# Performance work log

Hardware: AMD Instinct MI355X
Metric: run time of the kernel (lower is better)

The kernel has to match this reference:

```python
import jax, jax.numpy as jnp
import numpy as np

DIM, H, HD = 512, 8, 64
N_BANK = 4096
EPS = 1e-5


def layernorm(x, g, b):
    m = jnp.mean(x, axis=-1, keepdims=True)
    v = jnp.mean(jnp.square(x - m), axis=-1, keepdims=True)
    return (x - m) * jax.lax.rsqrt(v + EPS) * g + b


def setup_inputs() -> dict:
    key = jax.random.key(0)
    ks = jax.random.split(key, 8)
    # xavier_uniform bound for square (512,512) linears
    bound = float(np.sqrt(6.0 / (DIM + DIM)))
    inp = {
        "x_q": jax.random.normal(ks[0], (32, 128, DIM), jnp.float32),
        "x_k": jax.random.normal(ks[1], (N_BANK, DIM), jnp.float32),
        "x_v": jax.random.normal(ks[2], (N_BANK, DIM), jnp.float32),
        "Wq": jax.random.uniform(ks[3], (DIM, DIM), jnp.float32, -bound, bound),
        "Wk": jax.random.uniform(ks[4], (DIM, DIM), jnp.float32, -bound, bound),
        "Wv": jax.random.uniform(ks[5], (DIM, DIM), jnp.float32, -bound, bound),
        "Wproj": jax.random.uniform(ks[6], (DIM, DIM), jnp.float32, -bound, bound),
        "qn_g": jnp.ones((HD,), jnp.float32),
        "qn_b": jnp.zeros((HD,), jnp.float32),
        "kn_g": jnp.ones((HD,), jnp.float32),
        "kn_b": jnp.zeros((HD,), jnp.float32),
        "n_g": jnp.ones((DIM,), jnp.float32),
        "n_b": jnp.zeros((DIM,), jnp.float32),
    }
    return inp


def reference(x_q, x_k, x_v, Wq, Wk, Wv, Wproj, qn_g, qn_b, kn_g, kn_b, n_g, n_b):
    B, S, D = x_q.shape
    N = x_k.shape[0]
    scale = HD ** (-0.5)
    # Linear layers (torch: y = x @ W.T)
    q = jnp.einsum('bsd,od->bso', x_q, Wq).reshape(B, S, H, HD).transpose(0, 2, 1, 3)  # (B,H,S,hd)
    k = jnp.einsum('nd,od->no', x_k, Wk).reshape(N, H, HD).transpose(1, 0, 2)          # (H,N,hd)
    v = jnp.einsum('nd,od->no', x_v, Wv).reshape(N, H, HD).transpose(1, 0, 2)          # (H,N,hd)
    # per-head qk layernorm
    q = layernorm(q, qn_g, qn_b) * scale
    k = layernorm(k, kn_g, kn_b)
    # cross-attention to shared bank (K/V have no batch dim)
    attn = jnp.einsum('bhsd,hnd->bhsn', q, k)          # (B,H,S,N)
    attn = jax.nn.softmax(attn, axis=-1)
    x = jnp.einsum('bhsn,hnd->bhsd', attn, v)          # (B,H,S,hd)
    x = x.transpose(0, 2, 1, 3).reshape(B, S, D)
    x = layernorm(x, n_g, n_b)
    x = jnp.einsum('bsd,od->bso', x, Wproj)
    return x
```

## Files before the change

kernel.cpp:

```cpp
#include <hip/hip_runtime.h>
#include <hip/hip_bf16.h>
#include <math.h>

#define DIM 512
#define NHEAD 8
#define HD 64
#define NBANK 4096
#define NQROWS 4096
#define EPS 1e-5f
#define QSCALE 0.125f
#define PART_ELEMS (NQROWS * DIM)

typedef __attribute__((ext_vector_type(4))) float floatx4;
typedef __attribute__((ext_vector_type(8))) short short8;

__device__ __forceinline__ unsigned short f2bf(float f) {
    unsigned int u = __float_as_uint(f);
    u += 0x7fffu + ((u >> 16) & 1u);
    return (unsigned short)(u >> 16);
}
__device__ __forceinline__ float bf2f(unsigned short h) {
    return __uint_as_float(((unsigned int)h) << 16);
}
__device__ __forceinline__ unsigned int pk2(float a, float b) {
    union { __hip_bfloat162 h; unsigned int u; } cvt;
    cvt.h = __float22bfloat162_rn(make_float2(a, b));
    return cvt.u;
}

__global__ __launch_bounds__(256) void qkv_kernel(
    const float* __restrict__ xq, const float* __restrict__ xk, const float* __restrict__ xv,
    const float* __restrict__ Wqp, const float* __restrict__ Wkp, const float* __restrict__ Wvp,
    const float* __restrict__ qg, const float* __restrict__ qbeta,
    const float* __restrict__ kg, const float* __restrict__ kbeta,
    unsigned short* __restrict__ Qb, unsigned short* __restrict__ Kb,
    unsigned short* __restrict__ VTb)
{
    __shared__ short8 smem[1536];
    short8* as = smem;
    short8* bs = smem + 512;
    const int tid  = threadIdx.x;
    const int w    = tid >> 6, lane = tid & 63, m = lane & 15, q = lane >> 4;
    const int wr   = w & 1, wc = w >> 1;
    const int row0 = blockIdx.x * 64;
    const int mat  = blockIdx.y >> 2;
    const int col0 = (blockIdx.y & 3) * 128;
    const float* X = (mat == 0) ? xq : (mat == 1) ? xk : xv;
    const float* W = (mat == 0) ? Wqp : (mat == 1) ? Wkp : Wvp;

    floatx4 acc[2][4];
    #pragma unroll
    for (int mt = 0; mt < 2; ++mt)
        #pragma unroll
        for (int nt = 0; nt < 4; ++nt) acc[mt][nt] = (floatx4){0.f, 0.f, 0.f, 0.f};

    for (int k0 = 0; k0 < DIM; k0 += 64) {
        #pragma unroll
        for (int p = 0; p < 6; ++p) {
            const int idx = tid + p * 256;
            if (idx < 512) {
                const int row = idx >> 3, seg = idx & 7;
                const float4* pa = (const float4*)(X + (size_t)(row0 + row) * DIM + k0 + seg * 8);
                const float4 a0 = pa[0], a1 = pa[1];
                union { short8 v; unsigned int u[4]; } ta;
                ta.u[0] = pk2(a0.x, a0.y); ta.u[1] = pk2(a0.z, a0.w);
                ta.u[2] = pk2(a1.x, a1.y); ta.u[3] = pk2(a1.z, a1.w);
                as[row * 8 + (seg ^ (row & 7))] = ta.v;
            } else {
                const int j = idx - 512;
                const int row = j >> 3, seg = j & 7;
                const float4* pb = (const float4*)(W + (size_t)(col0 + row) * DIM + k0 + seg * 8);
                const float4 b0 = pb[0], b1 = pb[1];
                union { short8 v; unsigned int u[4]; } tb;
                tb.u[0] = pk2(b0.x, b0.y); tb.u[1] = pk2(b0.z, b0.w);
                tb.u[2] = pk2(b1.x, b1.y); tb.u[3] = pk2(b1.z, b1.w);
                bs[row * 8 + (seg ^ (row & 7))] = tb.v;
            }
        }
        __syncthreads();
        #pragma unroll
        for (int s = 0; s < 2; ++s) {
            short8 af[2], bfr[4];
            #pragma unroll
            for (int mt = 0; mt < 2; ++mt)
                af[mt] = as[(wr * 32 + mt * 16 + m) * 8 + ((s * 4 + q) ^ (m & 7))];
            #pragma unroll
            for (int nt = 0; nt < 4; ++nt)
                bfr[nt] = bs[(wc * 64 + nt * 16 + m) * 8 + ((s * 4 + q) ^ (m & 7))];
            #pragma unroll
            for (int mt = 0; mt < 2; ++mt)
                #pragma unroll
                for (int nt = 0; nt < 4; ++nt)
                    acc[mt][nt] = __builtin_amdgcn_mfma_f32_16x16x32_bf16(af[mt], bfr[nt], acc[mt][nt], 0, 0, 0);
        }
        __syncthreads();
    }

    if (mat < 2) {
        const float* g = (mat == 0) ? qg : kg;
        const float* be = (mat == 0) ? qbeta : kbeta;
        unsigned short* Y = (mat == 0) ? Qb : Kb;
        float gv[4], bv[4];
        #pragma unroll
        for (int nt = 0; nt < 4; ++nt) { gv[nt] = g[nt * 16 + m]; bv[nt] = be[nt * 16 + m]; }
        #pragma unroll
        for (int mt = 0; mt < 2; ++mt) {
            #pragma unroll
            for (int r = 0; r < 4; ++r) {
                float s = 0.f, sq = 0.f;
                #pragma unroll
                for (int nt = 0; nt < 4; ++nt) { const float v = acc[mt][nt][r]; s += v; sq += v * v; }
                s  += __shfl_xor(s, 1);  s  += __shfl_xor(s, 2);  s  += __shfl_xor(s, 4);  s  += __shfl_xor(s, 8);
                sq += __shfl_xor(sq, 1); sq += __shfl_xor(sq, 2); sq += __shfl_xor(sq, 4); sq += __shfl_xor(sq, 8);
                const float mean = s * (1.f / HD);
                const float var  = sq * (1.f / HD) - mean * mean;
                const float rr   = rsqrtf(var + EPS);
                const int grow = row0 + wr * 32 + mt * 16 + q * 4 + r;
                #pragma unroll
                for (int nt = 0; nt < 4; ++nt) {
                    float v = (acc[mt][nt][r] - mean) * rr * gv[nt] + bv[nt];
                    if (mat == 0) v *= QSCALE;
                    Y[(size_t)grow * DIM + col0 + wc * 64 + nt * 16 + m] = f2bf(v);
                }
            }
        }
    } else {
        unsigned short* vt = (unsigned short*)smem;
        #pragma unroll
        for (int mt = 0; mt < 2; ++mt)
            #pragma unroll
            for (int nt = 0; nt < 4; ++nt) {
                const int c  = wc * 64 + nt * 16 + m;
                const int rw = wr * 32 + mt * 16 + q * 4;
                *(unsigned int*)(vt + c * 88 + rw)     = pk2(acc[mt][nt][0], acc[mt][nt][1]);
                *(unsigned int*)(vt + c * 88 + rw + 2) = pk2(acc[mt][nt][2], acc[mt][nt][3]);
            }
        __syncthreads();
        #pragma unroll
        for (int p = 0; p < 4; ++p) {
            const int idx = tid + p * 256;
            const int c = idx >> 3, sg = idx & 7;
            *(short8*)(VTb + (size_t)(col0 + c) * NBANK + row0 + sg * 8) =
                *(const short8*)(vt + c * 88 + sg * 8);
        }
    }
}

__global__ __launch_bounds__(256) void attn_kernel(
    const unsigned short* __restrict__ Qb, const unsigned short* __restrict__ Kb,
    const unsigned short* __restrict__ VTb, unsigned short* __restrict__ AOp,
    float* __restrict__ sums)
{
    __shared__ short8 ks [512];
    __shared__ short8 vts[512];
    __shared__ short8 ps [512];
    const int tid  = threadIdx.x;
    const int w    = tid >> 6;
    const int lane = tid & 63;
    const int m    = lane & 15;
    const int q    = lane >> 4;
    const int h    = blockIdx.x & 7;
    const int row0 = (blockIdx.x >> 3) * 64;
    const int part = blockIdx.y;
    const int base0 = part * 1024;

    short8 qf[2];
    #pragma unroll
    for (int s = 0; s < 2; ++s)
        qf[s] = *(const short8*)(Qb + (size_t)(row0 + w * 16 + m) * DIM + h * HD + s * 32 + q * 8);

    floatx4 of[4];
    float sump[4];
    #pragma unroll
    for (int t = 0; t < 4; ++t) of[t] = (floatx4){0.f, 0.f, 0.f, 0.f};
    #pragma unroll
    for (int r = 0; r < 4; ++r) sump[r] = 0.f;

    unsigned short* psu = (unsigned short*)ps;

    for (int base = base0; base < base0 + 1024; base += 64) {
        __syncthreads();
        #pragma unroll
        for (int it = 0; it < 2; ++it) {
            const int idx = tid + it * 256;
            const int n = idx >> 3, seg = idx & 7, sw = seg ^ (n & 7);
            ks [n * 8 + sw] = *(const short8*)(Kb  + (size_t)(base + n) * DIM  + h * HD + seg * 8);
            vts[n * 8 + sw] = *(const short8*)(VTb + (size_t)(h * HD + n) * NBANK + base + seg * 8);
        }
        __syncthreads();

        floatx4 sc[4];
        #pragma unroll
        for (int t = 0; t < 4; ++t) sc[t] = (floatx4){0.f, 0.f, 0.f, 0.f};
        #pragma unroll
        for (int s = 0; s < 2; ++s) {
            #pragma unroll
            for (int t = 0; t < 4; ++t) {
                const short8 kf = ks[(t * 16 + m) * 8 + ((s * 4 + q) ^ (m & 7))];
                sc[t] = __builtin_amdgcn_mfma_f32_16x16x32_bf16(qf[s], kf, sc[t], 0, 0, 0);
            }
        }

        #pragma unroll
        for (int t = 0; t < 4; ++t) {
            #pragma unroll
            for (int r = 0; r < 4; ++r) {
                const float p = __expf(sc[t][r]);
                sump[r] += p;
                const int row  = q * 4 + r;
                const int colb = t * 2 + (m >> 3);
                psu[(w * 16 + row) * 64 + ((colb ^ (row & 7)) * 8) + (m & 7)] = f2bf(p);
            }
        }

        short8 pf[2];
        #pragma unroll
        for (int s = 0; s < 2; ++s)
            pf[s] = ps[(w * 16 + m) * 8 + ((s * 4 + q) ^ (m & 7))];
        #pragma unroll
        for (int s = 0; s < 2; ++s) {
            #pragma unroll
            for (int t = 0; t < 4; ++t) {
                const short8 vf = vts[(t * 16 + m) * 8 + ((s * 4 + q) ^ (m & 7))];
                of[t] = __builtin_amdgcn_mfma_f32_16x16x32_bf16(pf[s], vf, of[t], 0, 0, 0);
            }
        }
    }

    #pragma unroll
    for (int r = 0; r < 4; ++r) {
        float s = sump[r];
        s += __shfl_xor(s, 1); s += __shfl_xor(s, 2);
        s += __shfl_xor(s, 4); s += __shfl_xor(s, 8);
        sump[r] = s;
    }
    if (m == 0) {
        #pragma unroll
        for (int r = 0; r < 4; ++r)
            sums[((size_t)part * NQROWS + row0 + w * 16 + q * 4 + r) * NHEAD + h] = sump[r];
    }
    #pragma unroll
    for (int t = 0; t < 4; ++t) {
        #pragma unroll
        for (int r = 0; r < 4; ++r) {
            AOp[(size_t)part * PART_ELEMS +
                (size_t)(row0 + w * 16 + q * 4 + r) * DIM + h * HD + t * 16 + m] = f2bf(of[t][r]);
        }
    }
}

__global__ __launch_bounds__(256) void combine_kernel(
    const unsigned short* __restrict__ AOp, const float* __restrict__ sums,
    unsigned short* __restrict__ AO, float* __restrict__ meanv, float* __restrict__ rstdv)
{
    __shared__ float rs[256], rq[256];
    const int tid = threadIdx.x;
    const int row = blockIdx.x * 2 + (tid >> 7);
    const int t   = tid & 127;
    const int h   = t >> 4;

    float stot = 0.f;
    #pragma unroll
    for (int p = 0; p < 4; ++p)
        stot += sums[((size_t)p * NQROWS + row) * NHEAD + h];

    float o[4] = {0.f, 0.f, 0.f, 0.f};
    #pragma unroll
    for (int p = 0; p < 4; ++p) {
        const ushort4 u = *(const ushort4*)(AOp + (size_t)p * PART_ELEMS + (size_t)row * DIM + t * 4);
        o[0] += bf2f(u.x); o[1] += bf2f(u.y); o[2] += bf2f(u.z); o[3] += bf2f(u.w);
    }
    const float inv = 1.0f / stot;
    float v0 = o[0] * inv, v1 = o[1] * inv, v2 = o[2] * inv, v3 = o[3] * inv;

    uint2 packed;
    packed.x = pk2(v0, v1); packed.y = pk2(v2, v3);
    *(uint2*)(AO + (size_t)row * DIM + t * 4) = packed;

    rs[tid] = v0 + v1 + v2 + v3;
    rq[tid] = v0 * v0 + v1 * v1 + v2 * v2 + v3 * v3;
    __syncthreads();
    #pragma unroll
    for (int off = 64; off > 0; off >>= 1) {
        if (t < off) { rs[tid] += rs[tid + off]; rq[tid] += rq[tid + off]; }
        __syncthreads();
    }
    if (t == 0) {
        const float mean = rs[tid] * (1.f / DIM);
        const float var  = rq[tid] * (1.f / DIM) - mean * mean;
        meanv[row] = mean;
        rstdv[row] = rsqrtf(var + EPS);
    }
}

__global__ __launch_bounds__(256) void final_kernel(
    const unsigned short* __restrict__ AO, const float* __restrict__ W,
    const float* __restrict__ meanv, const float* __restrict__ rstdv,
    const float* __restrict__ g, const float* __restrict__ be,
    float* __restrict__ out)
{
    __shared__ short8 fs[1024];
    __shared__ float gls[512], bls[512];
    const int tid  = threadIdx.x;
    const int w    = tid >> 6, lane = tid & 63, m = lane & 15, q = lane >> 4;
    const int row0 = blockIdx.x * 64;
    const int col0 = blockIdx.y * 64;

    #pragma unroll
    for (int i = 0; i < 2; ++i) { gls[tid + i * 256] = g[tid + i * 256]; bls[tid + i * 256] = be[tid + i * 256]; }

    floatx4 acc[4];
    #pragma unroll
    for (int mt = 0; mt < 4; ++mt) acc[mt] = (floatx4){0.f, 0.f, 0.f, 0.f};
    __syncthreads();

    for (int k0 = 0; k0 < DIM; k0 += 64) {
        #pragma unroll
        for (int p = 0; p < 4; ++p) {
            const int idx = tid + p * 256;
            if (idx < 512) {
                const int row = idx >> 3, seg = idx & 7;
                const short8 a = *(const short8*)(AO + (size_t)(row0 + row) * DIM + k0 + seg * 8);
                const float mm = meanv[row0 + row], rr = rstdv[row0 + row];
                const float* gp = gls + k0 + seg * 8;
                const float* bp = bls + k0 + seg * 8;
                float v[8];
                #pragma unroll
                for (int j = 0; j < 8; ++j)
                    v[j] = (bf2f((unsigned short)a[j]) - mm) * rr * gp[j] + bp[j];
                union { short8 s; unsigned int u[4]; } ta;
                ta.u[0] = pk2(v[0], v[1]); ta.u[1] = pk2(v[2], v[3]);
                ta.u[2] = pk2(v[4], v[5]); ta.u[3] = pk2(v[6], v[7]);
                fs[row * 8 + (seg ^ (row & 7))] = ta.s;
            } else {
                const int j = idx - 512;
                const int row = j >> 3, seg = j & 7;
                const float4* pb = (const float4*)(W + (size_t)(col0 + row) * DIM + k0 + seg * 8);
                const float4 b0 = pb[0], b1 = pb[1];
                union { short8 s; unsigned int u[4]; } tb;
                tb.u[0] = pk2(b0.x, b0.y); tb.u[1] = pk2(b0.z, b0.w);
                tb.u[2] = pk2(b1.x, b1.y); tb.u[3] = pk2(b1.z, b1.w);
                fs[512 + row * 8 + (seg ^ (row & 7))] = tb.s;
            }
        }
        __syncthreads();
        #pragma unroll
        for (int s = 0; s < 2; ++s) {
            short8 af[4];
            #pragma unroll
            for (int mt = 0; mt < 4; ++mt)
                af[mt] = fs[(mt * 16 + m) * 8 + ((s * 4 + q) ^ (m & 7))];
            const short8 bfr = fs[512 + (w * 16 + m) * 8 + ((s * 4 + q) ^ (m & 7))];
            #pragma unroll
            for (int mt = 0; mt < 4; ++mt)
                acc[mt] = __builtin_amdgcn_mfma_f32_16x16x32_bf16(af[mt], bfr, acc[mt], 0, 0, 0);
        }
        __syncthreads();
    }

    #pragma unroll
    for (int mt = 0; mt < 4; ++mt)
        #pragma unroll
        for (int r = 0; r < 4; ++r)
            out[(size_t)(row0 + mt * 16 + q * 4 + r) * DIM + col0 + w * 16 + m] = acc[mt][r];
}

extern "C" void kernel_launch(void* const* d_in, const int* in_sizes, int n_in,
                              void* d_out, int out_size, void* d_ws, size_t ws_size,
                              hipStream_t stream)
{
    const float* x_q = (const float*)d_in[0];
    const float* x_k = (const float*)d_in[1];
    const float* x_v = (const float*)d_in[2];
    const float* Wq  = (const float*)d_in[3];
    const float* Wk  = (const float*)d_in[4];
    const float* Wv  = (const float*)d_in[5];
    const float* Wp  = (const float*)d_in[6];
    const float* qg  = (const float*)d_in[7];
    const float* qb  = (const float*)d_in[8];
    const float* kg  = (const float*)d_in[9];
    const float* kb  = (const float*)d_in[10];
    const float* ng  = (const float*)d_in[11];
    const float* nb  = (const float*)d_in[12];
    float* out = (float*)d_out;

    unsigned short* Qb   = (unsigned short*)d_ws;
    unsigned short* Kb   = Qb  + (size_t)NQROWS * DIM;
    unsigned short* VTb  = Kb  + (size_t)NBANK * DIM;
    unsigned short* AOp  = VTb + (size_t)NBANK * DIM;
    float*          sums = (float*)(AOp + (size_t)4 * PART_ELEMS);
    float*          meanv = sums + (size_t)4 * NQROWS * NHEAD;
    float*          rstdv = meanv + NQROWS;
    unsigned short* AO   = Qb;

    qkv_kernel<<<dim3(64, 12), 256, 0, stream>>>(x_q, x_k, x_v, Wq, Wk, Wv,
                                                 qg, qb, kg, kb, Qb, Kb, VTb);
    attn_kernel<<<dim3(512, 4), 256, 0, stream>>>(Qb, Kb, VTb, AOp, sums);
    combine_kernel<<<NQROWS / 2, 256, 0, stream>>>(AOp, sums, AO, meanv, rstdv);
    final_kernel<<<dim3(64, 8), 256, 0, stream>>>(AO, Wp, meanv, rstdv, ng, nb, out);
}
```

Measured before the change: 194.0 us.

## Compute transposed scores in attention so P stays in registers, double query rows per block

The attention kernel now computes S^T (K as the A operand), so each lane's exp'd probabilities can be packed straight into the B-operand fragment for the PV MFMA. This removes the shared-memory round trip for P. Each wave handles 32 query rows instead of 16, which halves the grid and reuses every K/V tile across twice as many queries. V^T is loaded in a permuted order to match the new fragment layout, and the output is staged through LDS for coalesced 16-byte stores. The cost is higher register pressure and possibly lower occupancy, since the grid shrinks to 1024 blocks.

```diff
diff --git a/kernel.cpp b/kernel.cpp
--- a/kernel.cpp
+++ b/kernel.cpp
@@ -151,101 +151,138 @@
     const unsigned short* __restrict__ VTb, unsigned short* __restrict__ AOp,
     float* __restrict__ sums)
 {
-    __shared__ short8 ks [512];
-    __shared__ short8 vts[512];
-    __shared__ short8 ps [512];
+    __shared__ short8 smem[1024];
+    short8* ks  = smem;
+    short8* vts = smem + 512;
     const int tid  = threadIdx.x;
     const int w    = tid >> 6;
     const int lane = tid & 63;
     const int m    = lane & 15;
-    const int q    = lane >> 4;
+    const int Qd   = lane >> 4;
     const int h    = blockIdx.x & 7;
-    const int row0 = (blockIdx.x >> 3) * 64;
+    const int qg   = blockIdx.x >> 3;
+    const int row0 = qg * 128;
     const int part = blockIdx.y;
     const int base0 = part * 1024;
 
-    short8 qf[2];
-    #pragma unroll
-    for (int s = 0; s < 2; ++s)
-        qf[s] = *(const short8*)(Qb + (size_t)(row0 + w * 16 + m) * DIM + h * HD + s * 32 + q * 8);
-
-    floatx4 of[4];
-    float sump[4];
-    #pragma unroll
-    for (int t = 0; t < 4; ++t) of[t] = (floatx4){0.f, 0.f, 0.f, 0.f};
-    #pragma unroll
-    for (int r = 0; r < 4; ++r) sump[r] = 0.f;
-
-    unsigned short* psu = (unsigned short*)ps;
+    short8 qf[2][2];
+    #pragma unroll
+    for (int mt = 0; mt < 2; ++mt)
+        #pragma unroll
+        for (int s = 0; s < 2; ++s)
+            qf[mt][s] = *(const short8*)(Qb + (size_t)(row0 + w * 32 + mt * 16 + m) * DIM
+                                         + h * HD + s * 32 + Qd * 8);
+
+    floatx4 of[4][2];
+    float sump[2] = {0.f, 0.f};
+    #pragma unroll
+    for (int t = 0; t < 4; ++t)
+        #pragma unroll
+        for (int mt = 0; mt < 2; ++mt) of[t][mt] = (floatx4){0.f, 0.f, 0.f, 0.f};
 
     for (int base = base0; base < base0 + 1024; base += 64) {
         __syncthreads();
         #pragma unroll
         for (int it = 0; it < 2; ++it) {
             const int idx = tid + it * 256;
-            const int n = idx >> 3, seg = idx & 7, sw = seg ^ (n & 7);
-            ks [n * 8 + sw] = *(const short8*)(Kb  + (size_t)(base + n) * DIM  + h * HD + seg * 8);
-            vts[n * 8 + sw] = *(const short8*)(VTb + (size_t)(h * HD + n) * NBANK + base + seg * 8);
-        }
-        __syncthreads();
-
-        floatx4 sc[4];
-        #pragma unroll
-        for (int t = 0; t < 4; ++t) sc[t] = (floatx4){0.f, 0.f, 0.f, 0.f};
-        #pragma unroll
-        for (int s = 0; s < 2; ++s) {
+            const int n = idx >> 3, seg = idx & 7;
+            ks[n * 8 + (seg ^ (n & 7))] =
+                *(const short8*)(Kb + (size_t)(base + n) * DIM + h * HD + seg * 8);
+        }
+        #pragma unroll
+        for (int it = 0; it < 2; ++it) {
+            const int idx = tid + it * 256;
+            const int d = idx >> 3, g = idx & 7;
+            const unsigned short* vp = VTb + (size_t)(h * HD + d) * NBANK + base
+                                       + (g >> 2) * 32 + (g & 3) * 4;
+            const ushort4 lo = *(const ushort4*)(vp);
+            const ushort4 hi = *(const ushort4*)(vp + 16);
+            union { short8 v; ushort4 h4[2]; } tv;
+            tv.h4[0] = lo; tv.h4[1] = hi;
+            vts[d * 8 + (g ^ (d & 7))] = tv.v;
+        }
+        __syncthreads();
+
+        floatx4 st[4][2];
+        #pragma unroll
+        for (int t = 0; t < 4; ++t)
+            #pragma unroll
+            for (int mt = 0; mt < 2; ++mt) st[t][mt] = (floatx4){0.f, 0.f, 0.f, 0.f};
+        #pragma unroll
+        for (int s = 0; s < 2; ++s)
             #pragma unroll
             for (int t = 0; t < 4; ++t) {
-                const short8 kf = ks[(t * 16 + m) * 8 + ((s * 4 + q) ^ (m & 7))];
-                sc[t] = __builtin_amdgcn_mfma_f32_16x16x32_bf16(qf[s], kf, sc[t], 0, 0, 0);
-            }
-        }
-
-        #pragma unroll
-        for (int t = 0; t < 4; ++t) {
-            #pragma unroll
-            for (int r = 0; r < 4; ++r) {
-                const float p = __expf(sc[t][r]);
-                sump[r] += p;
-                const int row  = q * 4 + r;
-                const int colb = t * 2 + (m >> 3);
-                psu[(w * 16 + row) * 64 + ((colb ^ (row & 7)) * 8) + (m & 7)] = f2bf(p);
-            }
-        }
-
-        short8 pf[2];
-        #pragma unroll
-        for (int s = 0; s < 2; ++s)
-            pf[s] = ps[(w * 16 + m) * 8 + ((s * 4 + q) ^ (m & 7))];
-        #pragma unroll
-        for (int s = 0; s < 2; ++s) {
-            #pragma unroll
-            for (int t = 0; t < 4; ++t) {
-                const short8 vf = vts[(t * 16 + m) * 8 + ((s * 4 + q) ^ (m & 7))];
-                of[t] = __builtin_amdgcn_mfma_f32_16x16x32_bf16(pf[s], vf, of[t], 0, 0, 0);
-            }
-        }
-    }
-
-    #pragma unroll
-    for (int r = 0; r < 4; ++r) {
-        float s = sump[r];
-        s += __shfl_xor(s, 1); s += __shfl_xor(s, 2);
-        s += __shfl_xor(s, 4); s += __shfl_xor(s, 8);
-        sump[r] = s;
-    }
-    if (m == 0) {
-        #pragma unroll
-        for (int r = 0; r < 4; ++r)
-            sums[((size_t)part * NQROWS + row0 + w * 16 + q * 4 + r) * NHEAD + h] = sump[r];
-    }
-    #pragma unroll
-    for (int t = 0; t < 4; ++t) {
-        #pragma unroll
-        for (int r = 0; r < 4; ++r) {
-            AOp[(size_t)part * PART_ELEMS +
-                (size_t)(row0 + w * 16 + q * 4 + r) * DIM + h * HD + t * 16 + m] = f2bf(of[t][r]);
-        }
+                const short8 kf = ks[(t * 16 + m) * 8 + ((s * 4 + Qd) ^ (m & 7))];
+                #pragma unroll
+                for (int mt = 0; mt < 2; ++mt)
+                    st[t][mt] = __builtin_amdgcn_mfma_f32_16x16x32_bf16(kf, qf[mt][s], st[t][mt], 0, 0, 0);
+            }
+
+        float p[4][2][4];
+        #pragma unroll
+        for (int t = 0; t < 4; ++t)
+            #pragma unroll
+            for (int mt = 0; mt < 2; ++mt)
+                #pragma unroll
+                for (int r = 0; r < 4; ++r) {
+                    const float e = __expf(st[t][mt][r]);
+                    p[t][mt][r] = e;
+                    sump[mt] += e;
+                }
+        union { short8 v; unsigned int u[4]; } pf[2][2];
+        #pragma unroll
+        for (int mt = 0; mt < 2; ++mt)
+            #pragma unroll
+            for (int s2 = 0; s2 < 2; ++s2)
+                #pragma unroll
+                for (int u = 0; u < 4; ++u)
+                    pf[mt][s2].u[u] = pk2(p[s2 * 2 + (u >> 1)][mt][(u & 1) * 2],
+                                          p[s2 * 2 + (u >> 1)][mt][(u & 1) * 2 + 1]);
+
+        #pragma unroll
+        for (int s2 = 0; s2 < 2; ++s2)
+            #pragma unroll
+            for (int t2 = 0; t2 < 4; ++t2) {
+                const short8 vf = vts[(t2 * 16 + m) * 8 + ((s2 * 4 + Qd) ^ (m & 7))];
+                #pragma unroll
+                for (int mt = 0; mt < 2; ++mt)
+                    of[t2][mt] = __builtin_amdgcn_mfma_f32_16x16x32_bf16(vf, pf[mt][s2].v, of[t2][mt], 0, 0, 0);
+            }
+    }
+
+    #pragma unroll
+    for (int mt = 0; mt < 2; ++mt) {
+        float s = sump[mt];
+        s += __shfl_xor(s, 16);
+        s += __shfl_xor(s, 32);
+        sump[mt] = s;
+    }
+    if (Qd == 0) {
+        #pragma unroll
+        for (int mt = 0; mt < 2; ++mt)
+            sums[((size_t)part * NQROWS + row0 + w * 32 + mt * 16 + m) * NHEAD + h] = sump[mt];
+    }
+
+    __syncthreads();
+    unsigned int* ob = (unsigned int*)smem;
+    #pragma unroll
+    for (int t2 = 0; t2 < 4; ++t2)
+        #pragma unroll
+        for (int mt = 0; mt < 2; ++mt) {
+            const int q  = w * 32 + mt * 16 + m;
+            const int blk = t2 * 2 + (Qd >> 1);
+            const int sub = (Qd & 1) * 2;
+            const int bs  = (blk ^ (q & 7)) * 4;
+            ob[q * 32 + bs + sub]     = pk2(of[t2][mt][0], of[t2][mt][1]);
+            ob[q * 32 + bs + sub + 1] = pk2(of[t2][mt][2], of[t2][mt][3]);
+        }
+    __syncthreads();
+    #pragma unroll
+    for (int pp = 0; pp < 4; ++pp) {
+        const int idx = tid + pp * 256;
+        const int q = idx >> 3, sg = idx & 7;
+        *(short8*)(AOp + (size_t)part * PART_ELEMS + (size_t)(row0 + q) * DIM + h * HD + sg * 8) =
+            smem[q * 8 + (sg ^ (q & 7))];
     }
 }
 
@@ -395,7 +432,7 @@
 
     qkv_kernel<<<dim3(64, 12), 256, 0, stream>>>(x_q, x_k, x_v, Wq, Wk, Wv,
                                                  qg, qb, kg, kb, Qb, Kb, VTb);
-    attn_kernel<<<dim3(512, 4), 256, 0, stream>>>(Qb, Kb, VTb, AOp, sums);
+    attn_kernel<<<dim3(256, 4), 256, 0, stream>>>(Qb, Kb, VTb, AOp, sums);
     combine_kernel<<<NQROWS / 2, 256, 0, stream>>>(AOp, sums, AO, meanv, rstdv);
     final_kernel<<<dim3(64, 8), 256, 0, stream>>>(AO, Wp, meanv, rstdv, ng, nb, out);
 }
```

Result: slower. 206.5 us (+6.5%).
